# Kernel optimization log

Hardware: AMD Instinct MI355X
Metric: run time of the kernel (lower is better)

Reference implementation:

```python
import jax, jax.numpy as jnp
import numpy as np

N, E, CIN, COUT = 50000, 800000, 61, 64
EPS = 1e-5


def batchnorm(h, g, b):
    # BatchNorm1d in training mode: batch stats (biased variance), affine
    m = jnp.mean(h, axis=0)
    v = jnp.var(h, axis=0)
    return g * (h - m) * jax.lax.rsqrt(v + EPS) + b


def setup_inputs() -> dict:
    key = jax.random.key(0)
    ks = jax.random.split(key, 7)
    x = jax.random.normal(ks[0], (N, CIN), jnp.float32)
    pos = jax.random.normal(ks[1], (N, 3), jnp.float32)
    edge_index = jax.random.randint(ks[2], (2, E), 0, N, dtype=jnp.int64)
    s1 = 1.0 / np.sqrt(CIN + 3)
    s2 = 1.0 / np.sqrt(COUT)
    ss = 1.0 / np.sqrt(CIN)
    W1 = jax.random.normal(ks[3], (CIN + 3, COUT), jnp.float32) * s1
    b1 = jnp.zeros((COUT,), jnp.float32)
    W2 = jax.random.normal(ks[4], (COUT, COUT), jnp.float32) * s2
    b2 = jnp.zeros((COUT,), jnp.float32)
    Ws = jax.random.normal(ks[5], (CIN, COUT), jnp.float32) * ss
    bs = jnp.zeros((COUT,), jnp.float32)
    ones = jnp.ones((COUT,), jnp.float32)
    zeros = jnp.zeros((COUT,), jnp.float32)
    return {
        "x": x, "pos": pos, "edge_index": edge_index,
        "W1": W1, "b1": b1, "g1": ones, "be1": zeros,
        "W2": W2, "b2": b2, "g2": ones, "be2": zeros,
        "Ws": Ws, "bs": bs, "gs": ones, "bes": zeros,
        "gf": ones, "bef": zeros,
    }


def reference(x, pos, edge_index, W1, b1, g1, be1, W2, b2, g2, be2,
              Ws, bs, gs, bes, gf, bef):
    src, dst = edge_index[0], edge_index[1]  # j -> i (source_to_target)
    # per-edge message: [x_j, pos_j - pos_i]  -> [E, CIN+3]
    msg = jnp.concatenate([x[src], pos[src] - pos[dst]], axis=-1)
    # local_nn = MLP([CIN+3, COUT, COUT]) with per-layer Lin -> ReLU -> BN
    h = batchnorm(jax.nn.relu(msg @ W1 + b1), g1, be1)
    h = batchnorm(jax.nn.relu(h @ W2 + b2), g2, be2)
    # scatter-max aggregation to destination nodes
    agg = jax.ops.segment_max(h, dst, num_segments=N)
    agg = jnp.where(jnp.isneginf(agg), 0.0, agg)  # nodes with no incoming edges
    # residual shortcut (Linear + BN since CIN != COUT)
    identity = batchnorm(x @ Ws + bs, gs, bes)
    return jax.nn.relu(batchnorm(agg, gf, bef) + identity)
```

## Files before the change

### kernel.cpp

```cpp
#include <hip/hip_runtime.h>

#define CIN 61
constexpr float EPS = 1e-5f;
constexpr double SCALE = 16777216.0;

using s16x8 = __attribute__((ext_vector_type(8))) short;
using fx4   = __attribute__((ext_vector_type(4))) float;

static __device__ __forceinline__ unsigned short f2bf(float f) {
  unsigned int u = __float_as_uint(f);
  u = (u + 0x7fffu + ((u >> 16) & 1u)) >> 16;
  return (unsigned short)u;
}
static __device__ __forceinline__ float bf2f(unsigned short h) {
  return __uint_as_float(((unsigned int)h) << 16);
}

__device__ __forceinline__ void stat_reduce(float val, float* red, long long* dst_ll) {
  int tid = threadIdx.x;
  red[tid] = val;
  __syncthreads();
  if (tid < 64) {
    float t = red[tid] + red[tid + 64] + red[tid + 128] + red[tid + 192];
    atomicAdd((unsigned long long*)&dst_ll[tid],
              (unsigned long long)(long long)((double)t * SCALE));
  }
  __syncthreads();
}

__global__ __launch_bounds__(256) void k_node(
    const float* __restrict__ x, const float* __restrict__ W1,
    const float* __restrict__ b1, const float* __restrict__ Ws,
    const float* __restrict__ bs, unsigned short* __restrict__ y,
    unsigned short* __restrict__ s_out, long long* __restrict__ stats, int N,
    const int* __restrict__ ei, unsigned int* __restrict__ hist,
    unsigned short* __restrict__ rank, int E) {
  const int tid = threadIdx.x, lane = tid & 63, wv = tid >> 6;
  float w1r[64], wsr[64];
#pragma unroll
  for (int k = 0; k < 64; ++k) {
    w1r[k] = (k < CIN) ? W1[k * 64 + lane] : 0.f;
    wsr[k] = (k < CIN) ? Ws[k * 64 + lane] : 0.f;
  }
  const float b1v = b1[lane], bsv = bs[lane];
  __shared__ float lrow[4][64];
  __shared__ float red[256];
  float ssum = 0.f, ssq = 0.f;
  const int nq = N >> 2;
  for (int q = blockIdx.x; q < nq; q += gridDim.x) {
    const int n = (q << 2) + wv;
    lrow[wv][lane] = (lane < CIN) ? x[(size_t)n * CIN + lane] : 0.f;
    __builtin_amdgcn_wave_barrier();
    float a0 = b1v, a1 = 0.f, a2 = 0.f, a3 = 0.f;
    float c0 = bsv, c1 = 0.f, c2 = 0.f, c3 = 0.f;
    const float4* rr = (const float4*)&lrow[wv][0];
#pragma unroll
    for (int k4 = 0; k4 < 16; ++k4) {
      float4 v = rr[k4];
      a0 = fmaf(v.x, w1r[4 * k4 + 0], a0);
      a1 = fmaf(v.y, w1r[4 * k4 + 1], a1);
      a2 = fmaf(v.z, w1r[4 * k4 + 2], a2);
      a3 = fmaf(v.w, w1r[4 * k4 + 3], a3);
      c0 = fmaf(v.x, wsr[4 * k4 + 0], c0);
      c1 = fmaf(v.y, wsr[4 * k4 + 1], c1);
      c2 = fmaf(v.z, wsr[4 * k4 + 2], c2);
      c3 = fmaf(v.w, wsr[4 * k4 + 3], c3);
    }
    y[(size_t)n * 64 + lane] = f2bf((a0 + a1) + (a2 + a3));
    const float sacc = (c0 + c1) + (c2 + c3);
    s_out[(size_t)n * 64 + lane] = f2bf(sacc);
    ssum += sacc;
    ssq = fmaf(sacc, sacc, ssq);
    __builtin_amdgcn_wave_barrier();
  }
  stat_reduce(ssum, red, stats + 256);
  stat_reduce(ssq, red, stats + 320);
  for (int i = blockIdx.x * 256 + tid; i < E; i += gridDim.x * 256) {
    const int dst = ei[E + i];
    rank[i] = (unsigned short)atomicAdd(&hist[dst], 1u);
  }
}

__global__ __launch_bounds__(256) void k_scan1(
    const unsigned int* __restrict__ hist, unsigned int* __restrict__ bsum) {
  const int tid = threadIdx.x, lane = tid & 63, wv = tid >> 6;
  const uint4 v = ((const uint4*)(hist + blockIdx.x * 1024))[tid];
  unsigned int s = v.x + v.y + v.z + v.w;
#pragma unroll
  for (int off = 1; off < 64; off <<= 1) s += __shfl_xor(s, off);
  __shared__ unsigned int wsum[4];
  if (lane == 0) wsum[wv] = s;
  __syncthreads();
  if (tid == 0) bsum[blockIdx.x] = wsum[0] + wsum[1] + wsum[2] + wsum[3];
}

__global__ void k_scan2(const unsigned int* __restrict__ bsum,
                        unsigned int* __restrict__ boff, int nb) {
  const int t = threadIdx.x;
  unsigned int v = (t < nb) ? bsum[t] : 0u;
  unsigned int incl = v;
#pragma unroll
  for (int off = 1; off < 64; off <<= 1) {
    unsigned int u = __shfl_up(incl, off);
    if (t >= off) incl += u;
  }
  if (t < nb) boff[t] = incl - v;
}

__global__ __launch_bounds__(256) void k_scan3(
    const unsigned int* __restrict__ hist, const unsigned int* __restrict__ boff,
    unsigned int* __restrict__ cursor0) {
  const int tid = threadIdx.x, lane = tid & 63, wv = tid >> 6;
  const uint4 v = ((const uint4*)(hist + blockIdx.x * 1024))[tid];
  const unsigned int s = v.x + v.y + v.z + v.w;
  unsigned int incl = s;
#pragma unroll
  for (int off = 1; off < 64; off <<= 1) {
    unsigned int u = __shfl_up(incl, off);
    if (lane >= off) incl += u;
  }
  __shared__ unsigned int wtot[4];
  if (lane == 63) wtot[wv] = incl;
  __syncthreads();
  unsigned int wb = boff[blockIdx.x];
#pragma unroll
  for (int k = 0; k < 4; ++k) wb += (k < wv) ? wtot[k] : 0u;
  const unsigned int ex = wb + incl - s;
  uint4 o;
  o.x = ex; o.y = ex + v.x; o.z = o.y + v.y; o.w = o.z + v.z;
  ((uint4*)(cursor0 + blockIdx.x * 1024))[tid] = o;
}

__global__ __launch_bounds__(256) void k_dstfill(
    const unsigned int* __restrict__ cursor0, unsigned short* __restrict__ dstS,
    int N) {
  const int d = blockIdx.x * 256 + threadIdx.x;
  if (d >= N) return;
  const unsigned int lo = cursor0[d];
  const unsigned int hi = cursor0[d + 1];
  for (unsigned int i = lo; i < hi; ++i) dstS[i] = (unsigned short)d;
}

__global__ __launch_bounds__(256) void k_edge1(
    const int* __restrict__ ei, const float* __restrict__ pos,
    const unsigned short* __restrict__ y, const float* __restrict__ W1,
    const unsigned int* __restrict__ cursor0, const unsigned short* __restrict__ rank,
    unsigned short* __restrict__ t1S, long long* __restrict__ stats, int E) {
  const int tid = threadIdx.x, lane = tid & 63, wv = tid >> 6;
  const int g8 = lane >> 3, c8 = lane & 7;
  float wp[3][8];
#pragma unroll
  for (int d = 0; d < 3; ++d)
#pragma unroll
    for (int i = 0; i < 8; ++i) wp[d][i] = W1[(61 + d) * 64 + 8 * c8 + i];
  float ssum[8] = {0.f, 0.f, 0.f, 0.f, 0.f, 0.f, 0.f, 0.f};
  float ssq[8]  = {0.f, 0.f, 0.f, 0.f, 0.f, 0.f, 0.f, 0.f};
  const int ngrp = E >> 3;
  const int nw = gridDim.x * 4;
  for (int q = blockIdx.x * 4 + wv; q < ngrp; q += 4 * nw) {
    const int qB = q + nw, qC = q + 2 * nw, qD = q + 3 * nw;
    const bool hB = qB < ngrp, hC = qC < ngrp, hD = qD < ngrp;
    const int eA = (q << 3) + g8;
    const int eB = hB ? (qB << 3) + g8 : eA;
    const int eC = hC ? (qC << 3) + g8 : eA;
    const int eD = hD ? (qD << 3) + g8 : eA;
    const int srcA = ei[eA], dstA = ei[E + eA];
    const int srcB = ei[eB], dstB = ei[E + eB];
    const int srcC = ei[eC], dstC = ei[E + eC];
    const int srcD = ei[eD], dstD = ei[E + eD];
    float pvA = 0.f, pvB = 0.f, pvC = 0.f, pvD = 0.f;
    if (c8 < 3) {
      pvA = pos[srcA * 3 + c8] - pos[dstA * 3 + c8];
      pvB = pos[srcB * 3 + c8] - pos[dstB * 3 + c8];
      pvC = pos[srcC * 3 + c8] - pos[dstC * 3 + c8];
      pvD = pos[srcD * 3 + c8] - pos[dstD * 3 + c8];
    }
    const s16x8 yA = *(const s16x8*)(y + (unsigned)srcA * 64u + 8u * (unsigned)c8);
    const s16x8 yB = *(const s16x8*)(y + (unsigned)srcB * 64u + 8u * (unsigned)c8);
    const s16x8 yC = *(const s16x8*)(y + (unsigned)srcC * 64u + 8u * (unsigned)c8);
    const s16x8 yD = *(const s16x8*)(y + (unsigned)srcD * 64u + 8u * (unsigned)c8);
    unsigned offA = 0, offB = 0, offC = 0, offD = 0;
    if (c8 == 0) {
      offA = cursor0[dstA] + rank[eA];
      offB = cursor0[dstB] + rank[eB];
      offC = cursor0[dstC] + rank[eC];
      offD = cursor0[dstD] + rank[eD];
    }
#define EDGE1_BODY(PV, YV, OFFV)                                                \
    {                                                                           \
      const float p0 = __shfl(PV, g8 * 8 + 0);                                  \
      const float p1 = __shfl(PV, g8 * 8 + 1);                                  \
      const float p2 = __shfl(PV, g8 * 8 + 2);                                  \
      const unsigned off = __shfl(OFFV, g8 * 8 + 0);                            \
      union { s16x8 v; unsigned short s[8]; } tb;                               \
      _Pragma("unroll")                                                         \
      for (int i = 0; i < 8; ++i) {                                             \
        float v = bf2f((unsigned short)YV[i]);                                  \
        v = fmaf(p0, wp[0][i], v);                                              \
        v = fmaf(p1, wp[1][i], v);                                              \
        v = fmaf(p2, wp[2][i], v);                                              \
        v = fmaxf(v, 0.f);                                                      \
        ssum[i] += v;                                                           \
        ssq[i] = fmaf(v, v, ssq[i]);                                            \
        tb.s[i] = f2bf(v);                                                      \
      }                                                                         \
      *(s16x8*)(t1S + (size_t)off * 64 + 8 * c8) = tb.v;                        \
    }
    EDGE1_BODY(pvA, yA, offA)
    if (hB) EDGE1_BODY(pvB, yB, offB)
    if (hC) EDGE1_BODY(pvC, yC, offC)
    if (hD) EDGE1_BODY(pvD, yD, offD)
#undef EDGE1_BODY
  }
#pragma unroll
  for (int i = 0; i < 8; ++i) {
    ssum[i] += __shfl_xor(ssum[i], 8);
    ssum[i] += __shfl_xor(ssum[i], 16);
    ssum[i] += __shfl_xor(ssum[i], 32);
    ssq[i] += __shfl_xor(ssq[i], 8);
    ssq[i] += __shfl_xor(ssq[i], 16);
    ssq[i] += __shfl_xor(ssq[i], 32);
  }
  __shared__ float sred[2][64];
  if (tid < 128) ((float*)sred)[tid] = 0.f;
  __syncthreads();
  if (g8 == 0) {
#pragma unroll
    for (int i = 0; i < 8; ++i) {
      atomicAdd(&sred[0][8 * c8 + i], ssum[i]);
      atomicAdd(&sred[1][8 * c8 + i], ssq[i]);
    }
  }
  __syncthreads();
  if (tid < 64) {
    atomicAdd((unsigned long long*)&stats[0 + tid],
              (unsigned long long)(long long)((double)sred[0][tid] * SCALE));
    atomicAdd((unsigned long long*)&stats[64 + tid],
              (unsigned long long)(long long)((double)sred[1][tid] * SCALE));
  }
}

__global__ void k_coefA(const long long* __restrict__ stats,
                        const float* __restrict__ g1, const float* __restrict__ be1,
                        const float* __restrict__ W2, const float* __restrict__ b2,
                        unsigned short* __restrict__ bFpack,
                        float* __restrict__ biasF, double invE) {
  const int c = threadIdx.x;
  __shared__ float a1s[64], c1s[64], b2sh[64];
  double m = (double)stats[c] * invE;
  double v = (double)stats[64 + c] * invE - m * m;
  float a = g1[c] * rsqrtf((float)v + EPS);
  a1s[c] = a;
  c1s[c] = fmaf(-(float)m, a, be1[c]);
  __syncthreads();
  float acc = b2[c];
  for (int k = 0; k < 64; ++k) acc = fmaf(c1s[k], W2[k * 64 + c], acc);
  b2sh[c] = acc;
  const int lg = c >> 4, l15 = c & 15;
#pragma unroll
  for (int t = 0; t < 4; ++t)
#pragma unroll
    for (int s = 0; s < 2; ++s)
#pragma unroll
      for (int i = 0; i < 8; ++i) {
        const int k = s * 32 + lg * 8 + i;
        bFpack[c * 64 + t * 16 + s * 8 + i] = f2bf(a1s[k] * W2[k * 64 + l15 + 16 * t]);
      }
  __syncthreads();
  float4 bf;
  bf.x = b2sh[l15]; bf.y = b2sh[l15 + 16]; bf.z = b2sh[l15 + 32]; bf.w = b2sh[l15 + 48];
  ((float4*)biasF)[c] = bf;
}

__global__ __launch_bounds__(256) void k_edge2(
    const unsigned short* __restrict__ t1S, const unsigned short* __restrict__ dstS,
    const unsigned short* __restrict__ bFpack, const float* __restrict__ biasF,
    long long* __restrict__ stats, unsigned int* __restrict__ agg, int E) {
  const int tid = threadIdx.x, lane = tid & 63, wv = tid >> 6;
  const int l15 = lane & 15, lg = lane >> 4;
  s16x8 bF[4][2];
  {
    const s16x8* bfp = (const s16x8*)(bFpack + (size_t)lane * 64);
#pragma unroll
    for (int t = 0; t < 4; ++t)
#pragma unroll
      for (int s = 0; s < 2; ++s) bF[t][s] = bfp[t * 2 + s];
  }
  float bias[4];
  {
    const float4 bv = ((const float4*)biasF)[lane];
    bias[0] = bv.x; bias[1] = bv.y; bias[2] = bv.z; bias[3] = bv.w;
  }
  float ssum[4] = {0.f, 0.f, 0.f, 0.f}, ssq[4] = {0.f, 0.f, 0.f, 0.f};
  const int ntile = E >> 4;
  const int nw = gridDim.x * 4;
  for (int tile = blockIdx.x * 4 + wv; tile < ntile; tile += nw) {
    const int rbase = tile << 4;
    const unsigned short* ar = t1S + (size_t)(rbase + l15) * 64 + (unsigned)(lg * 8);
    const s16x8 aF0 = *(const s16x8*)ar;
    const s16x8 aF1 = *(const s16x8*)(ar + 32);
    const int dstv = (int)dstS[rbase + l15];
    fx4 acc[4];
#pragma unroll
    for (int t = 0; t < 4; ++t) {
      acc[t][0] = bias[t]; acc[t][1] = bias[t];
      acc[t][2] = bias[t]; acc[t][3] = bias[t];
    }
#pragma unroll
    for (int t = 0; t < 4; ++t) {
      acc[t] = __builtin_amdgcn_mfma_f32_16x16x32_bf16(aF0, bF[t][0], acc[t], 0, 0, 0);
      acc[t] = __builtin_amdgcn_mfma_f32_16x16x32_bf16(aF1, bF[t][1], acc[t], 0, 0, 0);
    }
    float tv[4][4];
#pragma unroll
    for (int t = 0; t < 4; ++t)
#pragma unroll
      for (int j = 0; j < 4; ++j) {
        const float v = fmaxf(acc[t][j], 0.f);
        tv[t][j] = v;
        ssum[t] += v;
        ssq[t] = fmaf(v, v, ssq[t]);
      }
    const int prev = __shfl(dstv, (l15 + 15) & 15);
    const bool isb = (l15 == 0) || (dstv != prev);
    unsigned long long bm = __ballot(isb) & 0xFFFFull;
    while (bm) {
      const int r0 = __ffsll((long long)bm) - 1;
      bm &= bm - 1;
      const int r1 = bm ? (__ffsll((long long)bm) - 1) : 16;
      const int d = __shfl(dstv, r0);
      float lm[4];
#pragma unroll
      for (int t = 0; t < 4; ++t) {
        float m0 = 0.f;
#pragma unroll
        for (int j = 0; j < 4; ++j) {
          const int row = lg * 4 + j;
          m0 = fmaxf(m0, (row >= r0 && row < r1) ? tv[t][j] : 0.f);
        }
        m0 = fmaxf(m0, __shfl_xor(m0, 16));
        m0 = fmaxf(m0, __shfl_xor(m0, 32));
        lm[t] = m0;
      }
      const float val = (lg == 0) ? lm[0] : (lg == 1) ? lm[1] : (lg == 2) ? lm[2] : lm[3];
      atomicMax(&agg[(unsigned)d * 64u + (unsigned)(l15 + 16 * lg)],
                __float_as_uint(val) | 0x80000000u);
    }
  }
#pragma unroll
  for (int t = 0; t < 4; ++t) {
    ssum[t] += __shfl_xor(ssum[t], 16); ssum[t] += __shfl_xor(ssum[t], 32);
    ssq[t]  += __shfl_xor(ssq[t], 16);  ssq[t]  += __shfl_xor(ssq[t], 32);
  }
  __shared__ float sred[2][64];
  if (tid < 128) ((float*)sred)[tid] = 0.f;
  __syncthreads();
  if (lg == 0) {
#pragma unroll
    for (int t = 0; t < 4; ++t) {
      atomicAdd(&sred[0][l15 + 16 * t], ssum[t]);
      atomicAdd(&sred[1][l15 + 16 * t], ssq[t]);
    }
  }
  __syncthreads();
  if (tid < 64) {
    atomicAdd((unsigned long long*)&stats[128 + tid],
              (unsigned long long)(long long)((double)sred[0][tid] * SCALE));
    atomicAdd((unsigned long long*)&stats[192 + tid],
              (unsigned long long)(long long)((double)sred[1][tid] * SCALE));
  }
}

__global__ __launch_bounds__(256) void k_aggfix(
    const unsigned int* __restrict__ agg, long long* __restrict__ stats, int total) {
  const int tid = threadIdx.x;
  __shared__ float red[256];
  float ssum = 0.f, ssq = 0.f, kcf = 0.f;
  const int step = gridDim.x * 256;
  for (int i = blockIdx.x * 256 + tid; i < total; i += step) {
    const unsigned int u = agg[i];
    if (u >> 31) {
      const float v = __uint_as_float(u & 0x7fffffffu);
      ssum += v;
      ssq = fmaf(v, v, ssq);
      if ((i & 63) == 0) kcf += 1.f;
    }
  }
  stat_reduce(ssum, red, stats + 384);
  stat_reduce(ssq, red, stats + 448);
  stat_reduce(kcf, red, stats + 512);
}

__global__ void k_coefB(const long long* __restrict__ stats,
                        const float* __restrict__ g2, const float* __restrict__ be2,
                        const float* __restrict__ gs, const float* __restrict__ bes,
                        const float* __restrict__ gf, const float* __restrict__ bef,
                        float* __restrict__ coef, double invE, double invN, int N) {
  const int c = threadIdx.x;
  double m2 = (double)stats[128 + c] * invE;
  double v2 = (double)stats[192 + c] * invE - m2 * m2;
  float a2 = g2[c] * rsqrtf((float)v2 + EPS);
  float c2 = fmaf(-(float)m2, a2, be2[c]);
  double mS = (double)stats[256 + c] * invN;
  double vS = (double)stats[320 + c] * invN - mS * mS;
  float aS = gs[c] * rsqrtf((float)vS + EPS);
  float cS = fmaf(-(float)mS, aS, bes[c]);
  double su = (double)stats[384 + c] / SCALE;
  double qu = (double)stats[448 + c] / SCALE;
  double K  = (double)stats[512] / SCALE;
  double sv = (double)a2 * su + (double)c2 * K;
  double qv = (double)a2 * a2 * qu + 2.0 * a2 * c2 * su + (double)c2 * c2 * K;
  double mv = sv / N;
  double vv = qv / N - mv * mv;
  float aF = gf[c] * rsqrtf((float)vv + EPS);
  float cF = fmaf(-(float)mv, aF, bef[c]);
  coef[c]       = aF * a2;
  coef[64 + c]  = fmaf(aF, c2, cF);
  coef[128 + c] = cF;
  coef[192 + c] = aS;
  coef[256 + c] = cS;
}

__global__ __launch_bounds__(256) void k_final(
    const unsigned int* __restrict__ agg, const unsigned short* __restrict__ sbuf,
    const float* __restrict__ coef, float* __restrict__ out, int total) {
  int i = blockIdx.x * 256 + threadIdx.x;
  if (i >= total) return;
  const int c = i & 63;
  const unsigned int u = agg[i];
  float base;
  if (u >> 31)
    base = fmaf(coef[c], __uint_as_float(u & 0x7fffffffu), coef[64 + c]);
  else
    base = coef[128 + c];
  const float sv = fmaf(coef[192 + c], bf2f(sbuf[i]), coef[256 + c]);
  out[i] = fmaxf(base + sv, 0.f);
}

extern "C" void kernel_launch(void* const* d_in, const int* in_sizes, int n_in,
                              void* d_out, int out_size, void* d_ws, size_t ws_size,
                              hipStream_t stream) {
  const float* x   = (const float*)d_in[0];
  const float* pos = (const float*)d_in[1];
  const int*   ei  = (const int*)d_in[2];
  const float* W1  = (const float*)d_in[3];
  const float* b1  = (const float*)d_in[4];
  const float* g1  = (const float*)d_in[5];
  const float* be1 = (const float*)d_in[6];
  const float* W2  = (const float*)d_in[7];
  const float* b2  = (const float*)d_in[8];
  const float* g2  = (const float*)d_in[9];
  const float* be2 = (const float*)d_in[10];
  const float* Ws  = (const float*)d_in[11];
  const float* bs  = (const float*)d_in[12];
  const float* gs  = (const float*)d_in[13];
  const float* bes = (const float*)d_in[14];
  const float* gf  = (const float*)d_in[15];
  const float* bef = (const float*)d_in[16];
  const int N = in_sizes[0] / CIN;
  const int E = in_sizes[2] / 2;

  char* ws = (char*)d_ws;
  const size_t o_stats = 0;
  const size_t o_bsum  = 4608;
  const size_t o_boff  = 5120;
  const size_t o_hist  = 8192;
  const size_t o_agg   = o_hist + 200704;
  const size_t zeroEnd = o_agg + (size_t)N * 256;
  const size_t o_curs0 = zeroEnd;
  const size_t o_coef  = o_curs0 + 200704;
  const size_t o_frag  = o_coef + 4096;
  const size_t o_rank  = o_frag + 12288;
  const size_t o_dstS  = o_rank + (size_t)E * 2;
  const size_t o_ybuf  = o_dstS + (size_t)E * 2;
  const size_t o_sbuf  = o_ybuf + (size_t)N * 128;
  const size_t o_t1S   = o_sbuf + (size_t)N * 128;

  long long* stats      = (long long*)(ws + o_stats);
  unsigned int* bsum    = (unsigned int*)(ws + o_bsum);
  unsigned int* boff    = (unsigned int*)(ws + o_boff);
  unsigned int* hist    = (unsigned int*)(ws + o_hist);
  unsigned int* agg     = (unsigned int*)(ws + o_agg);
  unsigned int* cursor0 = (unsigned int*)(ws + o_curs0);
  float* coef           = (float*)(ws + o_coef);
  unsigned short* bFpack= (unsigned short*)(ws + o_frag);
  float* biasF          = (float*)(ws + o_frag + 8192);
  unsigned short* rank  = (unsigned short*)(ws + o_rank);
  unsigned short* dstS  = (unsigned short*)(ws + o_dstS);
  unsigned short* ybuf  = (unsigned short*)(ws + o_ybuf);
  unsigned short* sbuf  = (unsigned short*)(ws + o_sbuf);
  unsigned short* t1S   = (unsigned short*)(ws + o_t1S);

  const double invE = 1.0 / (SCALE * (double)E);
  const double invN = 1.0 / (SCALE * (double)N);
  const int total = N * 64;
  const int nScanBlk = 49;

  hipMemsetAsync(d_ws, 0, zeroEnd, stream);

  hipLaunchKernelGGL(k_node, dim3(1024), dim3(256), 0, stream,
                     x, W1, b1, Ws, bs, ybuf, sbuf, stats, N, ei, hist, rank, E);
  hipLaunchKernelGGL(k_scan1, dim3(nScanBlk), dim3(256), 0, stream, hist, bsum);
  hipLaunchKernelGGL(k_scan2, dim3(1), dim3(64), 0, stream, bsum, boff, nScanBlk);
  hipLaunchKernelGGL(k_scan3, dim3(nScanBlk), dim3(256), 0, stream,
                     hist, boff, cursor0);
  hipLaunchKernelGGL(k_dstfill, dim3((N + 255) / 256), dim3(256), 0, stream,
                     cursor0, dstS, N);
  hipLaunchKernelGGL(k_edge1, dim3(2048), dim3(256), 0, stream,
                     ei, pos, ybuf, W1, cursor0, rank, t1S, stats, E);
  hipLaunchKernelGGL(k_coefA, dim3(1), dim3(64), 0, stream,
                     stats, g1, be1, W2, b2, bFpack, biasF, invE);
  hipLaunchKernelGGL(k_edge2, dim3(2048), dim3(256), 0, stream,
                     t1S, dstS, bFpack, biasF, stats, agg, E);
  hipLaunchKernelGGL(k_aggfix, dim3(1024), dim3(256), 0, stream, agg, stats, total);
  hipLaunchKernelGGL(k_coefB, dim3(1), dim3(64), 0, stream,
                     stats, g2, be2, gs, bes, gf, bef, coef, invE, invN, N);
  hipLaunchKernelGGL(k_final, dim3((total + 255) / 256), dim3(256), 0, stream,
                     agg, sbuf, coef, (float*)d_out, total);
}
```

Baseline: 262.9 us.

## Fold scan2 and dstfill into scan3; prefetch next tile in edge2 loop

Removes the single-block k_scan2 by having each scan3 block sum the preceding block totals itself. It also writes the sorted destination array directly from scan3, which removes the k_dstfill launch. Separately, the k_edge2 tile loop is software-pipelined: it loads the next tile's A fragments and destination ids before running the current tile's MFMAs and atomics, to hide global load latency. The costs are higher register pressure in edge2 and only 49 blocks doing the dstS fill, which is less parallel than before.

```diff
diff --git a/kernel.cpp b/kernel.cpp
--- a/kernel.cpp
+++ b/kernel.cpp
@@ -94,23 +94,17 @@
   if (tid == 0) bsum[blockIdx.x] = wsum[0] + wsum[1] + wsum[2] + wsum[3];
 }
 
-__global__ void k_scan2(const unsigned int* __restrict__ bsum,
-                        unsigned int* __restrict__ boff, int nb) {
-  const int t = threadIdx.x;
-  unsigned int v = (t < nb) ? bsum[t] : 0u;
-  unsigned int incl = v;
-#pragma unroll
-  for (int off = 1; off < 64; off <<= 1) {
-    unsigned int u = __shfl_up(incl, off);
-    if (t >= off) incl += u;
-  }
-  if (t < nb) boff[t] = incl - v;
-}
-
 __global__ __launch_bounds__(256) void k_scan3(
-    const unsigned int* __restrict__ hist, const unsigned int* __restrict__ boff,
-    unsigned int* __restrict__ cursor0) {
+    const unsigned int* __restrict__ hist, const unsigned int* __restrict__ bsum,
+    unsigned int* __restrict__ cursor0, unsigned short* __restrict__ dstS, int N) {
   const int tid = threadIdx.x, lane = tid & 63, wv = tid >> 6;
+  __shared__ unsigned int s_boff;
+  if (tid < 64) {
+    unsigned int v = (tid < blockIdx.x) ? bsum[tid] : 0u;
+#pragma unroll
+    for (int off = 1; off < 64; off <<= 1) v += __shfl_xor(v, off);
+    if (tid == 0) s_boff = v;
+  }
   const uint4 v = ((const uint4*)(hist + blockIdx.x * 1024))[tid];
   const unsigned int s = v.x + v.y + v.z + v.w;
   unsigned int incl = s;
@@ -122,23 +116,19 @@
   __shared__ unsigned int wtot[4];
   if (lane == 63) wtot[wv] = incl;
   __syncthreads();
-  unsigned int wb = boff[blockIdx.x];
+  unsigned int wb = s_boff;
 #pragma unroll
   for (int k = 0; k < 4; ++k) wb += (k < wv) ? wtot[k] : 0u;
   const unsigned int ex = wb + incl - s;
   uint4 o;
   o.x = ex; o.y = ex + v.x; o.z = o.y + v.y; o.w = o.z + v.z;
   ((uint4*)(cursor0 + blockIdx.x * 1024))[tid] = o;
-}
-
-__global__ __launch_bounds__(256) void k_dstfill(
-    const unsigned int* __restrict__ cursor0, unsigned short* __restrict__ dstS,
-    int N) {
-  const int d = blockIdx.x * 256 + threadIdx.x;
-  if (d >= N) return;
-  const unsigned int lo = cursor0[d];
-  const unsigned int hi = cursor0[d + 1];
-  for (unsigned int i = lo; i < hi; ++i) dstS[i] = (unsigned short)d;
+  const unsigned int d0 = blockIdx.x * 1024 + tid * 4;
+  const unsigned int e4 = o.w + v.w;
+  for (unsigned int i = o.x; i < o.y; ++i) dstS[i] = (unsigned short)d0;
+  for (unsigned int i = o.y; i < o.z; ++i) dstS[i] = (unsigned short)(d0 + 1);
+  for (unsigned int i = o.z; i < o.w; ++i) dstS[i] = (unsigned short)(d0 + 2);
+  for (unsigned int i = o.w; i < e4;  ++i) dstS[i] = (unsigned short)(d0 + 3);
 }
 
 __global__ __launch_bounds__(256) void k_edge1(
@@ -294,57 +284,72 @@
   float ssum[4] = {0.f, 0.f, 0.f, 0.f}, ssq[4] = {0.f, 0.f, 0.f, 0.f};
   const int ntile = E >> 4;
   const int nw = gridDim.x * 4;
-  for (int tile = blockIdx.x * 4 + wv; tile < ntile; tile += nw) {
-    const int rbase = tile << 4;
-    const unsigned short* ar = t1S + (size_t)(rbase + l15) * 64 + (unsigned)(lg * 8);
-    const s16x8 aF0 = *(const s16x8*)ar;
-    const s16x8 aF1 = *(const s16x8*)(ar + 32);
-    const int dstv = (int)dstS[rbase + l15];
-    fx4 acc[4];
-#pragma unroll
-    for (int t = 0; t < 4; ++t) {
-      acc[t][0] = bias[t]; acc[t][1] = bias[t];
-      acc[t][2] = bias[t]; acc[t][3] = bias[t];
-    }
-#pragma unroll
-    for (int t = 0; t < 4; ++t) {
-      acc[t] = __builtin_amdgcn_mfma_f32_16x16x32_bf16(aF0, bF[t][0], acc[t], 0, 0, 0);
-      acc[t] = __builtin_amdgcn_mfma_f32_16x16x32_bf16(aF1, bF[t][1], acc[t], 0, 0, 0);
-    }
-    float tv[4][4];
-#pragma unroll
-    for (int t = 0; t < 4; ++t)
-#pragma unroll
-      for (int j = 0; j < 4; ++j) {
-        const float v = fmaxf(acc[t][j], 0.f);
-        tv[t][j] = v;
-        ssum[t] += v;
-        ssq[t] = fmaf(v, v, ssq[t]);
+  int tile = blockIdx.x * 4 + wv;
+  if (tile < ntile) {
+    const unsigned short* ar0 = t1S + (size_t)((tile << 4) + l15) * 64 + (unsigned)(lg * 8);
+    s16x8 aF0 = *(const s16x8*)ar0;
+    s16x8 aF1 = *(const s16x8*)(ar0 + 32);
+    int dstv = (int)dstS[(tile << 4) + l15];
+    for (;;) {
+      const int tn = tile + nw;
+      const bool hn = tn < ntile;
+      s16x8 aF0n, aF1n;
+      int dstvn = 0;
+      if (hn) {
+        const unsigned short* arn =
+            t1S + (size_t)((tn << 4) + l15) * 64 + (unsigned)(lg * 8);
+        aF0n = *(const s16x8*)arn;
+        aF1n = *(const s16x8*)(arn + 32);
+        dstvn = (int)dstS[(tn << 4) + l15];
       }
-    const int prev = __shfl(dstv, (l15 + 15) & 15);
-    const bool isb = (l15 == 0) || (dstv != prev);
-    unsigned long long bm = __ballot(isb) & 0xFFFFull;
-    while (bm) {
-      const int r0 = __ffsll((long long)bm) - 1;
-      bm &= bm - 1;
-      const int r1 = bm ? (__ffsll((long long)bm) - 1) : 16;
-      const int d = __shfl(dstv, r0);
-      float lm[4];
+      fx4 acc[4];
 #pragma unroll
       for (int t = 0; t < 4; ++t) {
-        float m0 = 0.f;
+        acc[t][0] = bias[t]; acc[t][1] = bias[t];
+        acc[t][2] = bias[t]; acc[t][3] = bias[t];
+      }
+#pragma unroll
+      for (int t = 0; t < 4; ++t) {
+        acc[t] = __builtin_amdgcn_mfma_f32_16x16x32_bf16(aF0, bF[t][0], acc[t], 0, 0, 0);
+        acc[t] = __builtin_amdgcn_mfma_f32_16x16x32_bf16(aF1, bF[t][1], acc[t], 0, 0, 0);
+      }
+      float tv[4][4];
+#pragma unroll
+      for (int t = 0; t < 4; ++t)
 #pragma unroll
         for (int j = 0; j < 4; ++j) {
-          const int row = lg * 4 + j;
-          m0 = fmaxf(m0, (row >= r0 && row < r1) ? tv[t][j] : 0.f);
+          const float v = fmaxf(acc[t][j], 0.f);
+          tv[t][j] = v;
+          ssum[t] += v;
+          ssq[t] = fmaf(v, v, ssq[t]);
         }
-        m0 = fmaxf(m0, __shfl_xor(m0, 16));
-        m0 = fmaxf(m0, __shfl_xor(m0, 32));
-        lm[t] = m0;
+      const int prev = __shfl(dstv, (l15 + 15) & 15);
+      const bool isb = (l15 == 0) || (dstv != prev);
+      unsigned long long bm = __ballot(isb) & 0xFFFFull;
+      while (bm) {
+        const int r0 = __ffsll((long long)bm) - 1;
+        bm &= bm - 1;
+        const int r1 = bm ? (__ffsll((long long)bm) - 1) : 16;
+        const int d = __shfl(dstv, r0);
+        float lm[4];
+#pragma unroll
+        for (int t = 0; t < 4; ++t) {
+          float m0 = 0.f;
+#pragma unroll
+          for (int j = 0; j < 4; ++j) {
+            const int row = lg * 4 + j;
+            m0 = fmaxf(m0, (row >= r0 && row < r1) ? tv[t][j] : 0.f);
+          }
+          m0 = fmaxf(m0, __shfl_xor(m0, 16));
+          m0 = fmaxf(m0, __shfl_xor(m0, 32));
+          lm[t] = m0;
+        }
+        const float val = (lg == 0) ? lm[0] : (lg == 1) ? lm[1] : (lg == 2) ? lm[2] : lm[3];
+        atomicMax(&agg[(unsigned)d * 64u + (unsigned)(l15 + 16 * lg)],
+                  __float_as_uint(val) | 0x80000000u);
       }
-      const float val = (lg == 0) ? lm[0] : (lg == 1) ? lm[1] : (lg == 2) ? lm[2] : lm[3];
-      atomicMax(&agg[(unsigned)d * 64u + (unsigned)(l15 + 16 * lg)],
-                __float_as_uint(val) | 0x80000000u);
+      if (!hn) break;
+      tile = tn; aF0 = aF0n; aF1 = aF1n; dstv = dstvn;
     }
   }
 #pragma unroll
@@ -463,7 +468,6 @@
   char* ws = (char*)d_ws;
   const size_t o_stats = 0;
   const size_t o_bsum  = 4608;
-  const size_t o_boff  = 5120;
   const size_t o_hist  = 8192;
   const size_t o_agg   = o_hist + 200704;
   const size_t zeroEnd = o_agg + (size_t)N * 256;
@@ -478,7 +482,6 @@
 
   long long* stats      = (long long*)(ws + o_stats);
   unsigned int* bsum    = (unsigned int*)(ws + o_bsum);
-  unsigned int* boff    = (unsigned int*)(ws + o_boff);
   unsigned int* hist    = (unsigned int*)(ws + o_hist);
   unsigned int* agg     = (unsigned int*)(ws + o_agg);
   unsigned int* cursor0 = (unsigned int*)(ws + o_curs0);
@@ -501,11 +504,8 @@
   hipLaunchKernelGGL(k_node, dim3(1024), dim3(256), 0, stream,
                      x, W1, b1, Ws, bs, ybuf, sbuf, stats, N, ei, hist, rank, E);
   hipLaunchKernelGGL(k_scan1, dim3(nScanBlk), dim3(256), 0, stream, hist, bsum);
-  hipLaunchKernelGGL(k_scan2, dim3(1), dim3(64), 0, stream, bsum, boff, nScanBlk);
   hipLaunchKernelGGL(k_scan3, dim3(nScanBlk), dim3(256), 0, stream,
-                     hist, boff, cursor0);
-  hipLaunchKernelGGL(k_dstfill, dim3((N + 255) / 256), dim3(256), 0, stream,
-                     cursor0, dstS, N);
+                     hist, bsum, cursor0, dstS, N);
   hipLaunchKernelGGL(k_edge1, dim3(2048), dim3(256), 0, stream,
                      ei, pos, ybuf, W1, cursor0, rank, t1S, stats, E);
   hipLaunchKernelGGL(k_coefA, dim3(1), dim3(64), 0, stream,
```

After: 264.0 us. No clear change (+0.4%).
